# Performance work log

Measured on AMD Instinct MI355X. Metric: run time of the kernel, lower is better.

## Reference

```python
import jax, jax.numpy as jnp
import numpy as np

EPS = 1e-5
DIM = 128
SCALE = DIM ** (-0.5)


def setup_inputs() -> dict:
    key = jax.random.key(0)
    k1, k2, k3 = jax.random.split(key, 3)
    B, N, D = 2, 128 * 128, DIM
    Q = N // 4
    x = jax.random.normal(k1, (B, N, D), dtype=jnp.float32)
    gamma = jnp.ones((D,), dtype=jnp.float32)
    beta = jnp.zeros((D,), dtype=jnp.float32)
    queries = jax.random.normal(k2, (Q, D), dtype=jnp.float32)
    W = jax.random.normal(k3, (2 * D, D), dtype=jnp.float32) * (1.0 / np.sqrt(D))
    return {"x": x, "gamma": gamma, "beta": beta, "queries": queries, "W": W}


def reference(x, gamma, beta, queries, W):
    # LayerNorm over last dim (eps matches torch default 1e-5)
    mu = jnp.mean(x, axis=-1, keepdims=True)
    var = jnp.mean(jnp.square(x - mu), axis=-1, keepdims=True)
    xn = (x - mu) * jax.lax.rsqrt(var + EPS) * gamma + beta  # [B, N, D]
    # learned-query cross attention: sim = Q @ xn^T * scale -> softmax -> @ xn
    sim = jnp.einsum('qd,bnd->bqn', queries, xn) * SCALE     # [B, Q, N]
    attn = jax.nn.softmax(sim, axis=-1)
    out = jnp.einsum('bqn,bnd->bqd', attn, xn)               # [B, Q, D]
    # trailing linear: dim -> 2*dim, no bias
    return jnp.einsum('bqd,ed->bqe', out, W)                 # [B, Q, 2D]
```

## Files before the change

kernel.cpp:

```cpp
#include <hip/hip_runtime.h>
#include <stdint.h>

#define Nn 16384
#define Dd 128
#define Qq 4096
#define Ee 256
#define NSPLIT 8
#define NCHUNK 2048
#define KV 64
#define NITER 32

typedef __bf16 bf16x8 __attribute__((ext_vector_type(8)));
typedef float floatx4 __attribute__((ext_vector_type(4)));

__device__ __forceinline__ float fexp2(float x) {
#if __has_builtin(__builtin_amdgcn_exp2f)
  return __builtin_amdgcn_exp2f(x);
#else
  return exp2f(x);
#endif
}
__device__ __forceinline__ unsigned pk_bf(float lo, float hi) {
  return __builtin_amdgcn_perm(__float_as_uint(hi) + 0x8000u,
                               __float_as_uint(lo) + 0x8000u, 0x07060302u);
}
__device__ __forceinline__ unsigned short bf1(float f) {
  return (unsigned short)((__float_as_uint(f) + 0x8000u) >> 16);
}

__global__ __launch_bounds__(256) void k_lnt(
    const float* __restrict__ x, const float* __restrict__ gamma,
    const float* __restrict__ beta, const float* __restrict__ queries,
    const float* __restrict__ W, unsigned* __restrict__ xn,
    unsigned short* __restrict__ xnT, unsigned short* __restrict__ qb,
    unsigned short* __restrict__ wb) {
  __shared__ uint2 lds2[64 * 32];
  const int tid = threadIdx.x;
  const int bid = blockIdx.x;
  const int b = bid >> 8, n0 = (bid & 255) * 64;
  const int r = tid >> 2, qd = tid & 3;

  const float4* xp = (const float4*)(x + ((size_t)(b * Nn + n0 + r)) * Dd + qd * 32);
  float4 v[8];
  float s = 0.f, s2 = 0.f;
#pragma unroll
  for (int i = 0; i < 8; ++i) {
    v[i] = xp[i];
    s += (v[i].x + v[i].y) + (v[i].z + v[i].w);
    s2 += (v[i].x * v[i].x + v[i].y * v[i].y) + (v[i].z * v[i].z + v[i].w * v[i].w);
  }
  s += __shfl_xor(s, 1); s2 += __shfl_xor(s2, 1);
  s += __shfl_xor(s, 2); s2 += __shfl_xor(s2, 2);
  float mu = s * (1.0f / 128.0f);
  float var = s2 * (1.0f / 128.0f) - mu * mu;
  float rs = rsqrtf(var + 1e-5f);

  const float4* gp = (const float4*)(gamma + qd * 32);
  const float4* bp = (const float4*)(beta + qd * 32);
  unsigned pk[16];
#pragma unroll
  for (int i = 0; i < 8; ++i) {
    float4 g = gp[i], bt = bp[i];
    float y0 = (v[i].x - mu) * rs * g.x + bt.x;
    float y1 = (v[i].y - mu) * rs * g.y + bt.y;
    float y2 = (v[i].z - mu) * rs * g.z + bt.z;
    float y3 = (v[i].w - mu) * rs * g.w + bt.w;
    pk[2 * i] = pk_bf(y0, y1);
    pk[2 * i + 1] = pk_bf(y2, y3);
  }
  uint4* xo = (uint4*)(xn + ((size_t)(b * Nn + n0 + r)) * 64 + qd * 16);
#pragma unroll
  for (int i = 0; i < 4; ++i)
    xo[i] = make_uint4(pk[4 * i], pk[4 * i + 1], pk[4 * i + 2], pk[4 * i + 3]);
  const int rk = r & 31;
#pragma unroll
  for (int kk = 0; kk < 8; ++kk)
    lds2[r * 32 + ((qd * 8 + kk) ^ rk)] = make_uint2(pk[2 * kk], pk[2 * kk + 1]);
  __syncthreads();
  const int dq = tid >> 3, nc = tid & 7;
  uint2 U[8];
#pragma unroll
  for (int j = 0; j < 8; ++j) {
    int rr = nc * 8 + j;
    U[j] = lds2[rr * 32 + (dq ^ (rr & 31))];
  }
#pragma unroll
  for (int e = 0; e < 4; ++e) {
    unsigned a0 = (e & 2) ? U[0].y : U[0].x, a1 = (e & 2) ? U[1].y : U[1].x;
    unsigned a2 = (e & 2) ? U[2].y : U[2].x, a3 = (e & 2) ? U[3].y : U[3].x;
    unsigned a4 = (e & 2) ? U[4].y : U[4].x, a5 = (e & 2) ? U[5].y : U[5].x;
    unsigned a6 = (e & 2) ? U[6].y : U[6].x, a7 = (e & 2) ? U[7].y : U[7].x;
    unsigned sel = (e & 1) ? 0x07060302u : 0x05040100u;
    uint4 o;
    o.x = __builtin_amdgcn_perm(a1, a0, sel);
    o.y = __builtin_amdgcn_perm(a3, a2, sel);
    o.z = __builtin_amdgcn_perm(a5, a4, sel);
    o.w = __builtin_amdgcn_perm(a7, a6, sel);
    *(uint4*)(xnT + ((size_t)(b * Dd + dq * 4 + e)) * Nn + n0 + nc * 8) = o;
  }
  const float QSC = 0.08838834764831845f * 1.4426950408889634f;
  for (int idx = bid * 256 + tid; idx < Qq * Dd + Ee * Dd; idx += 512 * 256) {
    if (idx < Qq * Dd) qb[idx] = bf1(queries[idx] * QSC);
    else wb[idx - Qq * Dd] = bf1(W[idx - Qq * Dd]);
  }
}

__global__ __launch_bounds__(512, 4) void k_attn(
    const unsigned short* __restrict__ xn,
    const unsigned short* __restrict__ xnT,
    const unsigned short* __restrict__ qb,
    float* __restrict__ o_part,
    float* __restrict__ l_part) {
  __shared__ uint4 lds_x[1024];
  __shared__ uint4 lds_xt[1024];
  __shared__ char lds_p[16384];

  const int bid = blockIdx.x;
  const int split = bid & 7, qt = (bid >> 3) & 31, b = bid >> 8;
  const int tid = threadIdx.x;
  const int wave = tid >> 6, lane = tid & 63;
  const int col = lane & 15, quad = lane >> 4;
  const int cs = col & 7;
  const int qwbase = qt * 128 + wave * 16;

  bf16x8 qf[4];
#pragma unroll
  for (int s = 0; s < 4; ++s)
    qf[s] = *(const bf16x8*)(qb + (size_t)(qwbase + col) * Dd + s * 32 + quad * 8);

  const floatx4 fz = {0.f, 0.f, 0.f, 0.f};
  floatx4 O[8];
#pragma unroll
  for (int d = 0; d < 8; ++d) O[d] = fz;
  float lsum = 0.f;

  const uint4* gx = (const uint4*)(xn + (size_t)b * Nn * Dd);
  const uint4* gxt = (const uint4*)(xnT + (size_t)b * Dd * Nn);

  for (int i = 0; i < NITER; ++i) {
    const int nb = split * NCHUNK + i * KV;
#pragma unroll
    for (int p = 0; p < 2; ++p) {
      int u = p * 512 + tid;
      int rr = u >> 4, c = u & 15;
      lds_x[rr * 16 + (c ^ (rr & 7))] = gx[(size_t)(nb + rr) * 16 + c];
    }
#pragma unroll
    for (int p = 0; p < 2; ++p) {
      int u = p * 512 + tid;
      int d = u >> 3, c = u & 7;
      lds_xt[d * 8 + (c ^ (d & 7))] = gxt[(size_t)d * (Nn / 8) + (nb / 8) + c];
    }
    __syncthreads();

    floatx4 S[4];
#pragma unroll
    for (int mt = 0; mt < 4; ++mt) S[mt] = fz;
#pragma unroll
    for (int s = 0; s < 4; ++s)
#pragma unroll
      for (int mt = 0; mt < 4; ++mt) {
        bf16x8 ax = *(const bf16x8*)&lds_x[(16 * mt + col) * 16 + ((4 * s + quad) ^ cs)];
        S[mt] = __builtin_amdgcn_mfma_f32_16x16x32_bf16(ax, qf[s], S[mt], 0, 0, 0);
      }

#pragma unroll
    for (int mt = 0; mt < 4; ++mt) {
      float p0 = fexp2(S[mt][0]);
      float p1 = fexp2(S[mt][1]);
      float p2 = fexp2(S[mt][2]);
      float p3 = fexp2(S[mt][3]);
      lsum += (p0 + p1) + (p2 + p3);
      *(uint2*)(lds_p + wave * 2048 + col * 128 +
                (((2 * mt + (quad >> 1)) ^ cs) * 16) + (quad & 1) * 8) =
          make_uint2(pk_bf(p0, p1), pk_bf(p2, p3));
    }

#pragma unroll
    for (int s2 = 0; s2 < 2; ++s2) {
      bf16x8 ap = *(const bf16x8*)(lds_p + wave * 2048 + col * 128 +
                                   (((4 * s2 + quad) ^ cs) * 16));
#pragma unroll
      for (int dn = 0; dn < 8; ++dn) {
        bf16x8 bx = *(const bf16x8*)&lds_xt[(16 * dn + col) * 8 + ((4 * s2 + quad) ^ cs)];
        O[dn] = __builtin_amdgcn_mfma_f32_16x16x32_bf16(ap, bx, O[dn], 0, 0, 0);
      }
    }
    __syncthreads();
  }

  float lt = lsum + __shfl_xor(lsum, 16);
  lt += __shfl_xor(lt, 32);
  if (quad == 0)
    l_part[(size_t)(b * NSPLIT + split) * Qq + qwbase + col] = lt;
#pragma unroll
  for (int dn = 0; dn < 8; ++dn)
#pragma unroll
    for (int r = 0; r < 4; ++r) {
      int q = qwbase + quad * 4 + r;
      o_part[((size_t)(b * NSPLIT + split) * Qq + q) * Dd + dn * 16 + col] = O[dn][r];
    }
}

__global__ __launch_bounds__(256) void k_comb(
    const float* __restrict__ o_part, const float* __restrict__ l_part,
    const unsigned short* __restrict__ wb, float* __restrict__ out) {
  __shared__ unsigned short lds_a[64 * 136];
  __shared__ float lds_linv[64];
  const int bid = blockIdx.x;
  const int b = bid >> 6, qc = bid & 63;
  const int qbase = qc * 64;
  const int tid = threadIdx.x;
  const int wave = tid >> 6, lane = tid & 63;
  const int col = lane & 15, quad = lane >> 4;

  if (tid < 64) {
    float l = 0.f;
#pragma unroll
    for (int s = 0; s < 8; ++s)
      l += l_part[(size_t)(b * 8 + s) * Qq + qbase + tid];
    lds_linv[tid] = 1.0f / l;
  }
  __syncthreads();

#pragma unroll
  for (int i = 0; i < 8; ++i) {
    int idx = i * 256 + tid;
    int q = idx >> 5, d4 = idx & 31;
    float4 acc = make_float4(0.f, 0.f, 0.f, 0.f);
#pragma unroll
    for (int s = 0; s < 8; ++s) {
      float4 v = *(const float4*)(o_part + ((size_t)(b * 8 + s) * Qq + qbase + q) * Dd + d4 * 4);
      acc.x += v.x; acc.y += v.y; acc.z += v.z; acc.w += v.w;
    }
    float li = lds_linv[q];
    *(uint2*)((char*)lds_a + (size_t)q * 272 + d4 * 8) =
        make_uint2(pk_bf(acc.x * li, acc.y * li), pk_bf(acc.z * li, acc.w * li));
  }
  __syncthreads();

  bf16x8 af[4];
#pragma unroll
  for (int s = 0; s < 4; ++s)
    af[s] = *(const bf16x8*)&lds_a[(wave * 16 + col) * 136 + s * 32 + quad * 8];

  const floatx4 fz = {0.f, 0.f, 0.f, 0.f};
#pragma unroll
  for (int en = 0; en < 16; ++en) {
    floatx4 C = fz;
#pragma unroll
    for (int s = 0; s < 4; ++s) {
      bf16x8 bw = *(const bf16x8*)(wb + (size_t)(en * 16 + col) * Dd + s * 32 + quad * 8);
      C = __builtin_amdgcn_mfma_f32_16x16x32_bf16(af[s], bw, C, 0, 0, 0);
    }
#pragma unroll
    for (int r = 0; r < 4; ++r) {
      int q0 = qbase + wave * 16 + quad * 4 + r;
      out[((size_t)b * Qq + q0) * Ee + en * 16 + col] = C[r];
    }
  }
}

extern "C" void kernel_launch(void* const* d_in, const int* in_sizes, int n_in,
                              void* d_out, int out_size, void* d_ws, size_t ws_size,
                              hipStream_t stream) {
  const float* x = (const float*)d_in[0];
  const float* gamma = (const float*)d_in[1];
  const float* beta = (const float*)d_in[2];
  const float* queries = (const float*)d_in[3];
  const float* W = (const float*)d_in[4];
  float* out = (float*)d_out;

  char* w = (char*)d_ws;
  unsigned short* xn = (unsigned short*)(w);
  unsigned short* xnT = (unsigned short*)(w + 8388608);
  unsigned short* qb = (unsigned short*)(w + 16777216);
  unsigned short* wb = (unsigned short*)(w + 17825792);
  float* o_part = (float*)(w + 17891328);
  float* l_part = (float*)(w + 51445760);

  k_lnt<<<dim3(512), dim3(256), 0, stream>>>(x, gamma, beta, queries, W,
                                             (unsigned*)xn, xnT, qb, wb);
  k_attn<<<dim3(512), dim3(512), 0, stream>>>(xn, xnT, qb, o_part, l_part);
  k_comb<<<dim3(128), dim3(256), 0, stream>>>(o_part, l_part, wb, out);
}
```

Baseline: 185.6 us.

## Switch to 32x32 MFMA, direct global-to-LDS loads with pre-swizzled layouts

Moves the attention and output-projection matmuls from 16x16x32 to 32x32x16 bf16 MFMA tiles, with each wave handling 32 query rows and blocks shrunk to 256 threads. The LN kernel now writes xn and xnT already XOR-swizzled, so the attention kernel can stage tiles with global_load_lds straight into LDS instead of going through registers. The query/W bf16 conversion is vectorized to float4, and the combine kernel is retiled to 32-query blocks. The aim is fewer MFMA instructions, fewer LDS operand reads per FLOP and less VGPR staging traffic, at the cost of larger accumulator register footprint and lower occupancy.

```diff
diff --git a/kernel.cpp b/kernel.cpp
--- a/kernel.cpp
+++ b/kernel.cpp
@@ -11,7 +11,7 @@
 #define NITER 32
 
 typedef __bf16 bf16x8 __attribute__((ext_vector_type(8)));
-typedef float floatx4 __attribute__((ext_vector_type(4)));
+typedef float floatx16 __attribute__((ext_vector_type(16)));
 
 __device__ __forceinline__ float fexp2(float x) {
 #if __has_builtin(__builtin_amdgcn_exp2f)
@@ -24,8 +24,10 @@
   return __builtin_amdgcn_perm(__float_as_uint(hi) + 0x8000u,
                                __float_as_uint(lo) + 0x8000u, 0x07060302u);
 }
-__device__ __forceinline__ unsigned short bf1(float f) {
-  return (unsigned short)((__float_as_uint(f) + 0x8000u) >> 16);
+__device__ __forceinline__ void stage16(const void* g, void* lds_uniform) {
+  __builtin_amdgcn_global_load_lds(
+      (const __attribute__((address_space(1))) unsigned int*)g,
+      (__attribute__((address_space(3))) unsigned int*)lds_uniform, 16, 0, 0);
 }
 
 __global__ __launch_bounds__(256) void k_lnt(
@@ -34,7 +36,7 @@
     const float* __restrict__ W, unsigned* __restrict__ xn,
     unsigned short* __restrict__ xnT, unsigned short* __restrict__ qb,
     unsigned short* __restrict__ wb) {
-  __shared__ uint2 lds2[64 * 32];
+  __shared__ __align__(16) uint2 lds2[64 * 32];
   const int tid = threadIdx.x;
   const int bid = blockIdx.x;
   const int b = bid >> 8, n0 = (bid & 255) * 64;
@@ -61,17 +63,14 @@
 #pragma unroll
   for (int i = 0; i < 8; ++i) {
     float4 g = gp[i], bt = bp[i];
-    float y0 = (v[i].x - mu) * rs * g.x + bt.x;
-    float y1 = (v[i].y - mu) * rs * g.y + bt.y;
-    float y2 = (v[i].z - mu) * rs * g.z + bt.z;
-    float y3 = (v[i].w - mu) * rs * g.w + bt.w;
-    pk[2 * i] = pk_bf(y0, y1);
-    pk[2 * i + 1] = pk_bf(y2, y3);
-  }
-  uint4* xo = (uint4*)(xn + ((size_t)(b * Nn + n0 + r)) * 64 + qd * 16);
-#pragma unroll
-  for (int i = 0; i < 4; ++i)
-    xo[i] = make_uint4(pk[4 * i], pk[4 * i + 1], pk[4 * i + 2], pk[4 * i + 3]);
+    pk[2 * i] = pk_bf((v[i].x - mu) * rs * g.x + bt.x, (v[i].y - mu) * rs * g.y + bt.y);
+    pk[2 * i + 1] = pk_bf((v[i].z - mu) * rs * g.z + bt.z, (v[i].w - mu) * rs * g.w + bt.w);
+  }
+  unsigned* xrow = xn + ((size_t)(b * Nn + n0 + r)) * 64;
+#pragma unroll
+  for (int j = 0; j < 4; ++j)
+    *(uint4*)(xrow + (((qd * 4 + j) ^ (r & 7)) * 4)) =
+        make_uint4(pk[4 * j], pk[4 * j + 1], pk[4 * j + 2], pk[4 * j + 3]);
   const int rk = r & 31;
 #pragma unroll
   for (int kk = 0; kk < 8; ++kk)
@@ -86,6 +85,7 @@
   }
 #pragma unroll
   for (int e = 0; e < 4; ++e) {
+    int d = dq * 4 + e;
     unsigned a0 = (e & 2) ? U[0].y : U[0].x, a1 = (e & 2) ? U[1].y : U[1].x;
     unsigned a2 = (e & 2) ? U[2].y : U[2].x, a3 = (e & 2) ? U[3].y : U[3].x;
     unsigned a4 = (e & 2) ? U[4].y : U[4].x, a5 = (e & 2) ? U[5].y : U[5].x;
@@ -96,125 +96,139 @@
     o.y = __builtin_amdgcn_perm(a3, a2, sel);
     o.z = __builtin_amdgcn_perm(a5, a4, sel);
     o.w = __builtin_amdgcn_perm(a7, a6, sel);
-    *(uint4*)(xnT + ((size_t)(b * Dd + dq * 4 + e)) * Nn + n0 + nc * 8) = o;
+    *(uint4*)(xnT + ((size_t)(b * Dd + d)) * Nn + n0 + (nc ^ (d & 7)) * 8) = o;
   }
   const float QSC = 0.08838834764831845f * 1.4426950408889634f;
-  for (int idx = bid * 256 + tid; idx < Qq * Dd + Ee * Dd; idx += 512 * 256) {
-    if (idx < Qq * Dd) qb[idx] = bf1(queries[idx] * QSC);
-    else wb[idx - Qq * Dd] = bf1(W[idx - Qq * Dd]);
-  }
-}
-
-__global__ __launch_bounds__(512, 4) void k_attn(
+  const int total4 = (Qq * Dd + Ee * Dd) / 4;
+  for (int u = bid * 256 + tid; u < total4; u += 512 * 256) {
+    if (u < Qq * Dd / 4) {
+      float4 v4 = ((const float4*)queries)[u];
+      ((uint2*)qb)[u] = make_uint2(pk_bf(v4.x * QSC, v4.y * QSC),
+                                   pk_bf(v4.z * QSC, v4.w * QSC));
+    } else {
+      float4 v4 = ((const float4*)W)[u - Qq * Dd / 4];
+      ((uint2*)wb)[u - Qq * Dd / 4] =
+          make_uint2(pk_bf(v4.x, v4.y), pk_bf(v4.z, v4.w));
+    }
+  }
+}
+
+__global__ __launch_bounds__(256, 2) void k_attn(
     const unsigned short* __restrict__ xn,
     const unsigned short* __restrict__ xnT,
     const unsigned short* __restrict__ qb,
     float* __restrict__ o_part,
     float* __restrict__ l_part) {
-  __shared__ uint4 lds_x[1024];
-  __shared__ uint4 lds_xt[1024];
-  __shared__ char lds_p[16384];
+  __shared__ __align__(16) char lds[49152];
+  char* lds_x = lds;
+  char* lds_xt = lds + 16384;
+  char* lds_p = lds + 32768;
 
   const int bid = blockIdx.x;
   const int split = bid & 7, qt = (bid >> 3) & 31, b = bid >> 8;
   const int tid = threadIdx.x;
   const int wave = tid >> 6, lane = tid & 63;
-  const int col = lane & 15, quad = lane >> 4;
-  const int cs = col & 7;
-  const int qwbase = qt * 128 + wave * 16;
-
-  bf16x8 qf[4];
-#pragma unroll
-  for (int s = 0; s < 4; ++s)
-    qf[s] = *(const bf16x8*)(qb + (size_t)(qwbase + col) * Dd + s * 32 + quad * 8);
-
-  const floatx4 fz = {0.f, 0.f, 0.f, 0.f};
-  floatx4 O[8];
-#pragma unroll
-  for (int d = 0; d < 8; ++d) O[d] = fz;
+  const int col = lane & 31, half = lane >> 5;
+  const int ck = col & 7;
+  const int qwbase = qt * 128 + wave * 32;
+
+  bf16x8 qf[8];
+#pragma unroll
+  for (int s = 0; s < 8; ++s)
+    qf[s] = *(const bf16x8*)(qb + (size_t)(qwbase + col) * Dd + s * 16 + half * 8);
+
+  const floatx16 fz = {0.f,0.f,0.f,0.f,0.f,0.f,0.f,0.f,0.f,0.f,0.f,0.f,0.f,0.f,0.f,0.f};
+  floatx16 O[4];
+#pragma unroll
+  for (int d = 0; d < 4; ++d) O[d] = fz;
   float lsum = 0.f;
 
-  const uint4* gx = (const uint4*)(xn + (size_t)b * Nn * Dd);
-  const uint4* gxt = (const uint4*)(xnT + (size_t)b * Dd * Nn);
+  const char* gx = (const char*)xn + (size_t)b * Nn * 256;
+  const char* gxt = (const char*)xnT + (size_t)b * Dd * Nn * 2;
+  char* ldsp_w = lds_p + wave * 4096;
 
   for (int i = 0; i < NITER; ++i) {
     const int nb = split * NCHUNK + i * KV;
-#pragma unroll
-    for (int p = 0; p < 2; ++p) {
-      int u = p * 512 + tid;
-      int rr = u >> 4, c = u & 15;
-      lds_x[rr * 16 + (c ^ (rr & 7))] = gx[(size_t)(nb + rr) * 16 + c];
-    }
-#pragma unroll
-    for (int p = 0; p < 2; ++p) {
-      int u = p * 512 + tid;
-      int d = u >> 3, c = u & 7;
-      lds_xt[d * 8 + (c ^ (d & 7))] = gxt[(size_t)d * (Nn / 8) + (nb / 8) + c];
+    const char* xsrc = gx + (size_t)nb * 256;
+#pragma unroll
+    for (int p = 0; p < 4; ++p) {
+      int m = wave * 4 + p;
+      stage16(xsrc + m * 1024 + lane * 16, lds_x + m * 1024);
+    }
+#pragma unroll
+    for (int p = 0; p < 4; ++p) {
+      int m = wave * 4 + p;
+      const char* g = gxt + (size_t)(m * 8 + (lane >> 3)) * (Nn * 2) +
+                      (size_t)nb * 2 + (lane & 7) * 16;
+      stage16(g, lds_xt + m * 1024);
     }
     __syncthreads();
 
-    floatx4 S[4];
-#pragma unroll
-    for (int mt = 0; mt < 4; ++mt) S[mt] = fz;
-#pragma unroll
-    for (int s = 0; s < 4; ++s)
-#pragma unroll
-      for (int mt = 0; mt < 4; ++mt) {
-        bf16x8 ax = *(const bf16x8*)&lds_x[(16 * mt + col) * 16 + ((4 * s + quad) ^ cs)];
-        S[mt] = __builtin_amdgcn_mfma_f32_16x16x32_bf16(ax, qf[s], S[mt], 0, 0, 0);
+    floatx16 S[2];
+    S[0] = fz; S[1] = fz;
+#pragma unroll
+    for (int s = 0; s < 8; ++s)
+#pragma unroll
+      for (int mt = 0; mt < 2; ++mt) {
+        bf16x8 ax = *(const bf16x8*)(lds_x + (32 * mt + col) * 256 +
+                                     (((2 * s + half) ^ ck) * 16));
+        S[mt] = __builtin_amdgcn_mfma_f32_32x32x16_bf16(ax, qf[s], S[mt], 0, 0, 0);
       }
 
 #pragma unroll
-    for (int mt = 0; mt < 4; ++mt) {
-      float p0 = fexp2(S[mt][0]);
-      float p1 = fexp2(S[mt][1]);
-      float p2 = fexp2(S[mt][2]);
-      float p3 = fexp2(S[mt][3]);
-      lsum += (p0 + p1) + (p2 + p3);
-      *(uint2*)(lds_p + wave * 2048 + col * 128 +
-                (((2 * mt + (quad >> 1)) ^ cs) * 16) + (quad & 1) * 8) =
-          make_uint2(pk_bf(p0, p1), pk_bf(p2, p3));
-    }
-
-#pragma unroll
-    for (int s2 = 0; s2 < 2; ++s2) {
-      bf16x8 ap = *(const bf16x8*)(lds_p + wave * 2048 + col * 128 +
-                                   (((4 * s2 + quad) ^ cs) * 16));
-#pragma unroll
-      for (int dn = 0; dn < 8; ++dn) {
-        bf16x8 bx = *(const bf16x8*)&lds_xt[(16 * dn + col) * 8 + ((4 * s2 + quad) ^ cs)];
-        O[dn] = __builtin_amdgcn_mfma_f32_16x16x32_bf16(ap, bx, O[dn], 0, 0, 0);
+    for (int mt = 0; mt < 2; ++mt)
+#pragma unroll
+      for (int t = 0; t < 4; ++t) {
+        float p0 = fexp2(S[mt][4 * t]);
+        float p1 = fexp2(S[mt][4 * t + 1]);
+        float p2 = fexp2(S[mt][4 * t + 2]);
+        float p3 = fexp2(S[mt][4 * t + 3]);
+        lsum += (p0 + p1) + (p2 + p3);
+        int w = 4 * mt + t;
+        *(uint2*)(ldsp_w + col * 128 + ((w ^ ck) * 16) + half * 8) =
+            make_uint2(pk_bf(p0, p1), pk_bf(p2, p3));
       }
+
+#pragma unroll
+    for (int s2 = 0; s2 < 4; ++s2) {
+      bf16x8 ap = *(const bf16x8*)(ldsp_w + col * 128 + (((2 * s2 + half) ^ ck) * 16));
+#pragma unroll
+      for (int dn = 0; dn < 4; ++dn) {
+        bf16x8 bx = *(const bf16x8*)(lds_xt + (32 * dn + col) * 128 +
+                                     (((2 * s2 + half) ^ ck) * 16));
+        O[dn] = __builtin_amdgcn_mfma_f32_32x32x16_bf16(ap, bx, O[dn], 0, 0, 0);
+      }
     }
     __syncthreads();
   }
 
-  float lt = lsum + __shfl_xor(lsum, 16);
-  lt += __shfl_xor(lt, 32);
-  if (quad == 0)
+  float lt = lsum + __shfl_xor(lsum, 32);
+  if (half == 0)
     l_part[(size_t)(b * NSPLIT + split) * Qq + qwbase + col] = lt;
-#pragma unroll
-  for (int dn = 0; dn < 8; ++dn)
-#pragma unroll
-    for (int r = 0; r < 4; ++r) {
-      int q = qwbase + quad * 4 + r;
-      o_part[((size_t)(b * NSPLIT + split) * Qq + q) * Dd + dn * 16 + col] = O[dn][r];
+  float* op = o_part + ((size_t)(b * NSPLIT + split) * Qq + qwbase) * Dd;
+#pragma unroll
+  for (int dn = 0; dn < 4; ++dn)
+#pragma unroll
+    for (int r = 0; r < 16; ++r) {
+      int q = (r & 3) + 8 * (r >> 2) + 4 * half;
+      op[(size_t)q * Dd + dn * 32 + col] = O[dn][r];
     }
 }
 
 __global__ __launch_bounds__(256) void k_comb(
     const float* __restrict__ o_part, const float* __restrict__ l_part,
     const unsigned short* __restrict__ wb, float* __restrict__ out) {
-  __shared__ unsigned short lds_a[64 * 136];
-  __shared__ float lds_linv[64];
+  __shared__ __align__(16) char lds_a[32 * 256];
+  __shared__ float lds_linv[32];
   const int bid = blockIdx.x;
-  const int b = bid >> 6, qc = bid & 63;
-  const int qbase = qc * 64;
+  const int b = bid >> 7, qc = bid & 127;
+  const int qbase = qc * 32;
   const int tid = threadIdx.x;
   const int wave = tid >> 6, lane = tid & 63;
-  const int col = lane & 15, quad = lane >> 4;
-
-  if (tid < 64) {
+  const int col = lane & 31, half = lane >> 5;
+  const int ck = col & 7;
+
+  if (tid < 32) {
     float l = 0.f;
 #pragma unroll
     for (int s = 0; s < 8; ++s)
@@ -224,7 +238,7 @@
   __syncthreads();
 
 #pragma unroll
-  for (int i = 0; i < 8; ++i) {
+  for (int i = 0; i < 4; ++i) {
     int idx = i * 256 + tid;
     int q = idx >> 5, d4 = idx & 31;
     float4 acc = make_float4(0.f, 0.f, 0.f, 0.f);
@@ -234,29 +248,35 @@
       acc.x += v.x; acc.y += v.y; acc.z += v.z; acc.w += v.w;
     }
     float li = lds_linv[q];
-    *(uint2*)((char*)lds_a + (size_t)q * 272 + d4 * 8) =
+    int w = d4 >> 1;
+    int pos = (w & 8) | ((w ^ (q & 7)) & 7);
+    *(uint2*)(lds_a + q * 256 + pos * 16 + (d4 & 1) * 8) =
         make_uint2(pk_bf(acc.x * li, acc.y * li), pk_bf(acc.z * li, acc.w * li));
   }
   __syncthreads();
 
-  bf16x8 af[4];
-#pragma unroll
-  for (int s = 0; s < 4; ++s)
-    af[s] = *(const bf16x8*)&lds_a[(wave * 16 + col) * 136 + s * 32 + quad * 8];
-
-  const floatx4 fz = {0.f, 0.f, 0.f, 0.f};
-#pragma unroll
-  for (int en = 0; en < 16; ++en) {
-    floatx4 C = fz;
-#pragma unroll
-    for (int s = 0; s < 4; ++s) {
-      bf16x8 bw = *(const bf16x8*)(wb + (size_t)(en * 16 + col) * Dd + s * 32 + quad * 8);
-      C = __builtin_amdgcn_mfma_f32_16x16x32_bf16(af[s], bw, C, 0, 0, 0);
-    }
-#pragma unroll
-    for (int r = 0; r < 4; ++r) {
-      int q0 = qbase + wave * 16 + quad * 4 + r;
-      out[((size_t)b * Qq + q0) * Ee + en * 16 + col] = C[r];
+  bf16x8 af[8];
+#pragma unroll
+  for (int s = 0; s < 8; ++s) {
+    int u = 2 * s + half;
+    int pos = (u & 8) | ((u ^ ck) & 7);
+    af[s] = *(const bf16x8*)(lds_a + col * 256 + pos * 16);
+  }
+
+  const floatx16 fz = {0.f,0.f,0.f,0.f,0.f,0.f,0.f,0.f,0.f,0.f,0.f,0.f,0.f,0.f,0.f,0.f};
+#pragma unroll
+  for (int et = 0; et < 2; ++et) {
+    floatx16 C = fz;
+    int e_row = wave * 64 + et * 32 + col;
+#pragma unroll
+    for (int s = 0; s < 8; ++s) {
+      bf16x8 bw = *(const bf16x8*)(wb + (size_t)e_row * Dd + s * 16 + half * 8);
+      C = __builtin_amdgcn_mfma_f32_32x32x16_bf16(af[s], bw, C, 0, 0, 0);
+    }
+#pragma unroll
+    for (int r = 0; r < 16; ++r) {
+      int q = qbase + (r & 3) + 8 * (r >> 2) + 4 * half;
+      out[((size_t)b * Qq + q) * Ee + wave * 64 + et * 32 + col] = C[r];
     }
   }
 }
@@ -281,6 +301,6 @@
 
   k_lnt<<<dim3(512), dim3(256), 0, stream>>>(x, gamma, beta, queries, W,
                                              (unsigned*)xn, xnT, qb, wb);
-  k_attn<<<dim3(512), dim3(512), 0, stream>>>(xn, xnT, qb, o_part, l_part);
-  k_comb<<<dim3(128), dim3(256), 0, stream>>>(o_part, l_part, wb, out);
-}
+  k_attn<<<dim3(512), dim3(256), 0, stream>>>(xn, xnT, qb, o_part, l_part);
+  k_comb<<<dim3(256), dim3(256), 0, stream>>>(o_part, l_part, wb, out);
+}
```

Result: faster. 168.1 us (-9.4%).
